# Performance work log

Measured on AMD Instinct MI355X. Metric: run time of the kernel, lower is better.

The kernel has to match this reference:

```python
import jax, jax.numpy as jnp
import numpy as np

B, T, D, H, L = 64, 512, 256, 512, 4


def setup_inputs() -> dict:
    key = jax.random.key(0)
    ks = jax.random.split(key, 1 + 2 * L)
    inp = {"x": jax.random.normal(ks[0], (B, T, D), dtype=jnp.float32)}
    s = 0.05
    for l in range(L):
        in_dim = D if l == 0 else H
        inp[f"W{l}"] = jax.random.normal(ks[1 + 2 * l], (4 * H, in_dim), dtype=jnp.float32) * s
        inp[f"U{l}"] = jax.random.normal(ks[2 + 2 * l], (4 * H, H), dtype=jnp.float32) * s
        inp[f"bw{l}"] = jnp.zeros((4 * H,), dtype=jnp.float32)
        inp[f"bu{l}"] = jnp.zeros((4 * H,), dtype=jnp.float32)
    return inp


def _lstm_forward(x, params):
    # x: [B, T, D]; params: list of (W [4H,in], U [4H,H], bw [4H], bu [4H])
    Bq = x.shape[0]
    h0 = [jnp.zeros((Bq, H), x.dtype) for _ in range(L)]
    c0 = [jnp.zeros((Bq, H), x.dtype) for _ in range(L)]

    def step(carry, x_t):
        hs, cs = carry
        new_h, new_c = [], []
        inp = x_t  # [B, in]
        for (W, U, bw, bu), h_i, c_i in zip(params, hs, cs):
            z = inp @ W.T + bw + h_i @ U.T + bu  # [B, 4H]
            f, i, o, g = jnp.split(z, 4, axis=-1)  # gate order f,i,o,g
            f = jax.nn.sigmoid(f)
            i = jax.nn.sigmoid(i)
            o = jax.nn.sigmoid(o)
            g = jnp.tanh(g)
            c_n = f * c_i + i * g
            h_n = o * jnp.tanh(c_n)
            new_h.append(h_n)
            new_c.append(c_n)
            inp = h_n
        return (new_h, new_c), inp

    (h_f, c_f), out = jax.lax.scan(step, (h0, c0), jnp.swapaxes(x, 0, 1))
    output = jnp.swapaxes(out, 0, 1)  # [B, T, H]
    return output, jnp.stack(h_f), jnp.stack(c_f)


def reference(x, W0, U0, bw0, bu0, W1, U1, bw1, bu1, W2, U2, bw2, bu2, W3, U3, bw3, bu3):
    params = [(W0, U0, bw0, bu0), (W1, U1, bw1, bu1), (W2, U2, bw2, bu2), (W3, U3, bw3, bu3)]
    return _lstm_forward(x, params)
```

## Files before the change

kernel.cpp:

```cpp
#include <hip/hip_runtime.h>

typedef __attribute__((ext_vector_type(8))) short bf16x8;
typedef __attribute__((ext_vector_type(4))) float f32x4;

#define WPL 32
#define NT 256
#define RING 8

__device__ __forceinline__ unsigned short f2bf(float f) {
  unsigned int u = __float_as_uint(f);
  u += 0x7FFFu + ((u >> 16) & 1u);
  return (unsigned short)(u >> 16);
}
__device__ __forceinline__ float sigmoid_fast(float x) {
  return __builtin_amdgcn_rcpf(1.0f + __builtin_amdgcn_exp2f(-1.4426950408889634f * x));
}
__device__ __forceinline__ float tanh_fast(float x) {
  return 1.0f - 2.0f * __builtin_amdgcn_rcpf(
                           1.0f + __builtin_amdgcn_exp2f(2.885390081777927f * x));
}
__device__ __forceinline__ void wait_vm0() {
  asm volatile("s_waitcnt vmcnt(0)" ::: "memory");
  __builtin_amdgcn_sched_barrier(0);
}
#define WAITVM(N)                                         \
  do {                                                    \
    asm volatile("s_waitcnt vmcnt(" #N ")" ::: "memory"); \
    __builtin_amdgcn_sched_barrier(0);                    \
  } while (0)

template <int MODE>
__device__ __forceinline__ void ldA(bf16x8& d, int voff, const unsigned short* base) {
  if constexpr (MODE == 0)
    asm volatile("global_load_dwordx4 %0, %1, %2"
                 : "=v"(d) : "v"(voff), "s"(base));
  else
    asm volatile("global_load_dwordx4 %0, %1, %2 sc0 sc1"
                 : "=v"(d) : "v"(voff), "s"(base));
}
__device__ __forceinline__ unsigned ld_flag(const unsigned* p) {
  unsigned v;
  asm volatile("global_load_dword %0, %1, off sc0 sc1\n\ts_waitcnt vmcnt(0)"
               : "=v"(v) : "v"(p) : "memory");
  return v;
}
__device__ __forceinline__ void st16_coh(void* p, f32x4 v) {
  asm volatile("global_store_dwordx4 %0, %1, off sc0 sc1" :: "v"(p), "v"(v) : "memory");
}
__device__ __forceinline__ void st4_coh(void* p, unsigned v) {
  asm volatile("global_store_dword %0, %1, off sc0 sc1" :: "v"(p), "v"(v) : "memory");
}


__global__ void cvt_x_kernel(const float* __restrict__ x,
                             unsigned short* __restrict__ xf) {
  int tid = blockIdx.x * 256 + threadIdx.x;
  int t     = tid >> 11;
  int inner = tid & 2047;
  int lane  = inner & 63;
  int bt    = (inner >> 6) & 3;
  int c     = inner >> 8;
  int b = bt * 16 + (lane & 15);
  int d = c * 32 + (lane >> 4) * 8;
  const float* s = x + ((size_t)b * 512 + t) * 256 + d;
  f32x4 v0 = *(const f32x4*)s;
  f32x4 v1 = *(const f32x4*)(s + 4);
  bf16x8 o;
  o[0] = (short)f2bf(v0[0]); o[1] = (short)f2bf(v0[1]);
  o[2] = (short)f2bf(v0[2]); o[3] = (short)f2bf(v0[3]);
  o[4] = (short)f2bf(v1[0]); o[5] = (short)f2bf(v1[1]);
  o[6] = (short)f2bf(v1[2]); o[7] = (short)f2bf(v1[3]);
  *(bf16x8*)(xf + (size_t)t * 16384 + (size_t)inner * 8) = o;
}

__global__ void cvt_w_kernel(const float* __restrict__ W,
                             const float* __restrict__ U,
                             unsigned short* __restrict__ dst,
                             int C2, int split) {
  int tid = blockIdx.x * 256 + threadIdx.x;
  int lane = tid & 63;
  int c    = (tid >> 6) % C2;
  int rest = tid / (64 * C2);
  int g = rest & 3;
  int w = rest >> 2;
  int row = g * 512 + w * 16 + (lane & 15);
  int k   = c * 32 + (lane >> 4) * 8;
  const float* s = (k < split) ? (W + (size_t)row * split + k)
                               : (U + (size_t)row * 512 + (k - split));
  f32x4 v0 = *(const f32x4*)s;
  f32x4 v1 = *(const f32x4*)(s + 4);
  bf16x8 o;
  o[0] = (short)f2bf(v0[0]); o[1] = (short)f2bf(v0[1]);
  o[2] = (short)f2bf(v0[2]); o[3] = (short)f2bf(v0[3]);
  o[4] = (short)f2bf(v1[0]); o[5] = (short)f2bf(v1[1]);
  o[6] = (short)f2bf(v1[2]); o[7] = (short)f2bf(v1[3]);
  *(bf16x8*)(dst + (size_t)tid * 8) = o;
}

__global__ void bias_kernel(const float* __restrict__ bw,
                            const float* __restrict__ bu,
                            float* __restrict__ dst) {
  int i = blockIdx.x * 256 + threadIdx.x;
  dst[i] = bw[i] + bu[i];
}

__global__ void zero_flags(unsigned int* __restrict__ p) {
  int i = blockIdx.x * 256 + threadIdx.x;
  p[i] = 0u;
}

template <int C1, int C2, int M1, int M2>
__device__ __forceinline__ void gemm_run(const unsigned short* __restrict__ a1,
                                         const unsigned short* __restrict__ a2,
                                         const char* bg0, const char* bg1,
                                         const char* bg2, const char* bg3,
                                         int voffA, f32x4 acc[4]) {
  constexpr int NP = C2 / 4;
  bf16x8 av[3][4];
  bf16x8 bb[2][4][4];
  const char* bgp[4] = {bg0, bg1, bg2, bg3};

  auto issueA_iter = [&](int cc, int s3, int i) {
    if (cc < C1)
      ldA<M1>(av[s3][i], voffA + cc * 4096, a1);
    else
      ldA<M2>(av[s3][i], voffA + (cc - C1) * 4096, a2);
  };
  auto issueA_phase = [&](int q) {
#pragma unroll
    for (int i = 0; i < 4; ++i) issueA_iter(4 * q + i, q % 3, i);
  };
  auto loadB_phase = [&](int q) {
#pragma unroll
    for (int i = 0; i < 4; ++i)
#pragma unroll
      for (int g = 0; g < 4; ++g)
        bb[q & 1][i][g] = *(const bf16x8*)(bgp[g] + (4 * q + i) * 1024);
  };

#pragma unroll
  for (int q = 0; q < 3; ++q)
    if (q < NP) issueA_phase(q);
  loadB_phase(0);

#pragma unroll
  for (int ph = 0; ph < NP; ++ph) {
    if (ph + 1 < NP) loadB_phase(ph + 1);
    if (ph < NP - 2) {
      WAITVM(8);
    } else if (ph == NP - 2) {
      WAITVM(4);
    } else {
      WAITVM(0);
    }
#pragma unroll
    for (int i = 0; i < 4; ++i)
#pragma unroll
      for (int g = 0; g < 4; ++g)
        acc[g] = __builtin_amdgcn_mfma_f32_16x16x32_bf16(av[ph % 3][i],
                                                         bb[ph & 1][i][g],
                                                         acc[g], 0, 0, 0);
    if (ph + 3 < NP) issueA_phase(ph + 3);
  }
}

__global__ void __launch_bounds__(NT, 1)
lstm_main(const unsigned short* __restrict__ xfrag,
          const unsigned short* __restrict__ wf0,
          const unsigned short* __restrict__ wf1,
          const unsigned short* __restrict__ wf2,
          const unsigned short* __restrict__ wf3,
          const float* __restrict__ bias,
          unsigned short* __restrict__ hbuf,
          unsigned int* __restrict__ flags,
          float* __restrict__ out) {
  extern __shared__ char smem[];

  const int bid   = blockIdx.x;
  const int layer = bid >> 5;
  const int w     = bid & 31;
  const int tid   = threadIdx.x;
  const int lane  = tid & 63;
  const int vm    = tid >> 6;
  const int l15   = lane & 15;
  const int lhi   = lane >> 4;
  const int hcol  = w * 16 + l15;
  const int C2r   = (layer == 0) ? 24 : 32;
  const int HOFF  = 4 * C2r * 64 * 16;

  const unsigned short* wfl =
      (layer == 0) ? wf0 : (layer == 1) ? wf1 : (layer == 2) ? wf2 : wf3;
  const unsigned short* wsl = wfl + (size_t)w * (4 * C2r * 64 * 8);

  for (int i = tid; i < 4 * C2r * 64; i += NT)
    *(f32x4*)(smem + (size_t)i * 16) = *(const f32x4*)(wsl + (size_t)i * 8);
  __syncthreads();

  const char* bg[4];
#pragma unroll
  for (int g = 0; g < 4; ++g) bg[g] = smem + ((size_t)g * C2r * 64 + lane) * 16;

  float bv[4];
#pragma unroll
  for (int g = 0; g < 4; ++g) bv[g] = bias[layer * 2048 + g * 512 + hcol];

  float creg[4];
#pragma unroll
  for (int r = 0; r < 4; ++r) creg[r] = 0.f;

  const int voffA = lane * 16 + vm * 1024;
  const int base_w = (w >> 1) * 2048 + (w & 1) * 256;

  const unsigned short* hprev =
      (layer == 0) ? nullptr : (hbuf + (size_t)(layer - 1) * RING * 32768);
  const unsigned short* hself = hbuf + (size_t)layer * RING * 32768;

  const int sb_bt = tid >> 5;
  const int sb_q  = (tid >> 4) & 1;
  const int sb_bl = tid & 15;
  const int slot_off = base_w + sb_bt * 512 + sb_q * 128 + sb_bl * 8;

  if (layer > 0 && vm == 0) {
    const unsigned* fp = flags;
    unsigned need = 0;
    if (lane < 32) {
      fp = flags + ((layer - 1) * 32 + lane) * 16;
      need = 1u;
    }
    while (true) {
      unsigned v = need ? ld_flag(fp) : 0u;
      if (__ballot(need && v < need) == 0) break;
      __builtin_amdgcn_s_sleep(1);
    }
  }
  __syncthreads();
  wait_vm0();

  for (int t = 0; t < 512; ++t) {
    const unsigned short* aW =
        (layer == 0) ? (xfrag + (size_t)t * 16384)
                     : (hprev + (size_t)(t & (RING - 1)) * 32768);
    const unsigned short* aU =
        hself + (size_t)((t - 1) & (RING - 1)) * 32768;

    f32x4 acc[4];
    const f32x4 z4 = {0.f, 0.f, 0.f, 0.f};
#pragma unroll
    for (int g = 0; g < 4; ++g) acc[g] = z4;

    if (t == 0) {
      if (layer == 0)
        gemm_run<8, 8, 0, 0>(aW, aW, bg[0], bg[1], bg[2], bg[3], voffA, acc);
      else
        gemm_run<16, 16, 2, 2>(aW, aW, bg[0], bg[1], bg[2], bg[3], voffA, acc);
    } else {
      if (layer == 0)
        gemm_run<8, 24, 0, 2>(aW, aU, bg[0], bg[1], bg[2], bg[3], voffA, acc);
      else
        gemm_run<16, 32, 2, 2>(aW, aU, bg[0], bg[1], bg[2], bg[3], voffA, acc);
    }

    float hreg[4], cnreg[4];
#pragma unroll
    for (int r = 0; r < 4; ++r) {
      float fg = sigmoid_fast(acc[0][r] + bv[0]);
      float ig = sigmoid_fast(acc[1][r] + bv[1]);
      float og = sigmoid_fast(acc[2][r] + bv[2]);
      float gg = tanh_fast(acc[3][r] + bv[3]);
      float cn = fg * creg[r] + ig * gg;
      creg[r] = cn;
      cnreg[r] = cn;
      float h = og * tanh_fast(cn);
      hreg[r] = h;
      *(unsigned short*)(smem + HOFF + (vm * 16 + lhi * 4 + r) * 32 + l15 * 2) =
          f2bf(h);
    }
    __syncthreads();

    if (tid < 128) {
      f32x4 hv = *(const f32x4*)(smem + HOFF + (sb_bt * 16 + sb_bl) * 32 + sb_q * 16);
      unsigned short* dst = hbuf +
          ((size_t)layer * RING + (t & (RING - 1))) * 32768 + slot_off;
      st16_coh(dst, hv);
      wait_vm0();
    }
    __syncthreads();
    if (tid == 0)
      st4_coh(flags + (layer * 32 + w) * 16, (unsigned)(t + 1));

    if (layer == 3) {
#pragma unroll
      for (int r = 0; r < 4; ++r) {
        int bidx = vm * 16 + lhi * 4 + r;
        out[(size_t)bidx * 262144 + (size_t)t * 512 + hcol] = hreg[r];
      }
    }
    if (t == 511) {
#pragma unroll
      for (int r = 0; r < 4; ++r) {
        int bidx = vm * 16 + lhi * 4 + r;
        out[16777216 + ((size_t)layer * 64 + bidx) * 512 + hcol] = hreg[r];
        out[16777216 + 131072 + ((size_t)layer * 64 + bidx) * 512 + hcol] = cnreg[r];
      }
    }

    if (t < 511) {
      if (vm == 0) {
        const unsigned* fp = flags;
        unsigned need = 0;
        if (lane < 32) {
          if (layer > 0) {
            fp = flags + ((layer - 1) * 32 + lane) * 16;
            need = (unsigned)(t + 2);
          }
        } else {
          fp = flags + (layer * 32 + (lane - 32)) * 16;
          need = (unsigned)(t + 1);
        }
        while (true) {
          unsigned v = need ? ld_flag(fp) : 0u;
          if (__ballot(need && v < need) == 0) break;
          __builtin_amdgcn_s_sleep(1);
        }
      } else if (vm == 1) {
        const unsigned* fp = flags;
        unsigned need = 0;
        if (lane < 32 && layer < 3 && (t + 1) >= RING) {
          fp = flags + ((layer + 1) * 32 + lane) * 16;
          need = (unsigned)(t + 2 - RING);
        }
        while (true) {
          unsigned v = need ? ld_flag(fp) : 0u;
          if (__ballot(need && v < need) == 0) break;
          __builtin_amdgcn_s_sleep(1);
        }
      }
      __syncthreads();
      wait_vm0();
    }
  }
}

extern "C" void kernel_launch(void* const* d_in, const int* in_sizes, int n_in,
                              void* d_out, int out_size, void* d_ws, size_t ws_size,
                              hipStream_t stream) {
  const float* x = (const float*)d_in[0];
  const float *W[4], *U[4], *bw[4], *bu[4];
  for (int l = 0; l < 4; ++l) {
    W[l]  = (const float*)d_in[1 + 4 * l];
    U[l]  = (const float*)d_in[2 + 4 * l];
    bw[l] = (const float*)d_in[3 + 4 * l];
    bu[l] = (const float*)d_in[4 + 4 * l];
  }

  char* ws = (char*)d_ws;
  unsigned short* xfrag = (unsigned short*)(ws + 0);
  unsigned short* wfr0  = (unsigned short*)(ws + 16777216);
  unsigned short* wfr1  = (unsigned short*)(ws + 19922944);
  unsigned short* wfr2  = (unsigned short*)(ws + 24117248);
  unsigned short* wfr3  = (unsigned short*)(ws + 28311552);
  float*          biasp = (float*)(ws + 32505856);
  unsigned short* hbuf  = (unsigned short*)(ws + 32538624);
  unsigned int*   flags = (unsigned int*)(ws + 34635776);
  float* out = (float*)d_out;

  cvt_x_kernel<<<4096, 256, 0, stream>>>(x, xfrag);
  cvt_w_kernel<<<768, 256, 0, stream>>>(W[0], U[0], wfr0, 24, 256);
  cvt_w_kernel<<<1024, 256, 0, stream>>>(W[1], U[1], wfr1, 32, 512);
  cvt_w_kernel<<<1024, 256, 0, stream>>>(W[2], U[2], wfr2, 32, 512);
  cvt_w_kernel<<<1024, 256, 0, stream>>>(W[3], U[3], wfr3, 32, 512);
  bias_kernel<<<8, 256, 0, stream>>>(bw[0], bu[0], biasp + 0 * 2048);
  bias_kernel<<<8, 256, 0, stream>>>(bw[1], bu[1], biasp + 1 * 2048);
  bias_kernel<<<8, 256, 0, stream>>>(bw[2], bu[2], biasp + 2 * 2048);
  bias_kernel<<<8, 256, 0, stream>>>(bw[3], bu[3], biasp + 3 * 2048);
  zero_flags<<<8, 256, 0, stream>>>(flags);

  hipFuncSetAttribute((const void*)lstm_main,
                      hipFuncAttributeMaxDynamicSharedMemorySize, 135168);
  lstm_main<<<dim3(4 * WPL), dim3(NT), 135168, stream>>>(
      xfrag, wfr0, wfr1, wfr2, wfr3, biasp, hbuf, flags, out);
}
```

Baseline: 1.891 ms.

## Halve block to two waves, each computing two 16-row M tiles

Cuts threads per block from 256 to 128, so each wave covers two 16-row batch tiles and reuses every LDS-loaded B fragment across two MFMAs. Per-wave LDS weight reads are roughly halved relative to compute, and block-wide syncs involve fewer waves on this latency-bound recurrent step. In exchange each wave does twice the MFMA and activation work per step with less parallelism to hide latency, and register pressure rises from the doubled accumulators and cell state.

```diff
diff --git a/kernel.cpp b/kernel.cpp
--- a/kernel.cpp
+++ b/kernel.cpp
@@ -4,7 +4,7 @@
 typedef __attribute__((ext_vector_type(4))) float f32x4;
 
 #define WPL 32
-#define NT 256
+#define NT 128
 #define RING 8
 
 __device__ __forceinline__ unsigned short f2bf(float f) {
@@ -114,28 +114,32 @@
                                          const unsigned short* __restrict__ a2,
                                          const char* bg0, const char* bg1,
                                          const char* bg2, const char* bg3,
-                                         int voffA, f32x4 acc[4]) {
-  constexpr int NP = C2 / 4;
-  bf16x8 av[3][4];
-  bf16x8 bb[2][4][4];
+                                         int voffA, f32x4 acc[2][4]) {
+  constexpr int NP = C2 / 2;
+  bf16x8 av[3][2][2];
+  bf16x8 bb[2][2][4];
   const char* bgp[4] = {bg0, bg1, bg2, bg3};
 
-  auto issueA_iter = [&](int cc, int s3, int i) {
-    if (cc < C1)
-      ldA<M1>(av[s3][i], voffA + cc * 4096, a1);
-    else
-      ldA<M2>(av[s3][i], voffA + (cc - C1) * 4096, a2);
-  };
   auto issueA_phase = [&](int q) {
 #pragma unroll
-    for (int i = 0; i < 4; ++i) issueA_iter(4 * q + i, q % 3, i);
+    for (int kk = 0; kk < 2; ++kk) {
+      int cc = 2 * q + kk;
+#pragma unroll
+      for (int m = 0; m < 2; ++m) {
+        int vo = voffA + m * 1024;
+        if (cc < C1)
+          ldA<M1>(av[q % 3][kk][m], vo + cc * 4096, a1);
+        else
+          ldA<M2>(av[q % 3][kk][m], vo + (cc - C1) * 4096, a2);
+      }
+    }
   };
   auto loadB_phase = [&](int q) {
 #pragma unroll
-    for (int i = 0; i < 4; ++i)
+    for (int kk = 0; kk < 2; ++kk)
 #pragma unroll
       for (int g = 0; g < 4; ++g)
-        bb[q & 1][i][g] = *(const bf16x8*)(bgp[g] + (4 * q + i) * 1024);
+        bb[q & 1][kk][g] = *(const bf16x8*)(bgp[g] + (2 * q + kk) * 1024);
   };
 
 #pragma unroll
@@ -154,12 +158,14 @@
       WAITVM(0);
     }
 #pragma unroll
-    for (int i = 0; i < 4; ++i)
-#pragma unroll
-      for (int g = 0; g < 4; ++g)
-        acc[g] = __builtin_amdgcn_mfma_f32_16x16x32_bf16(av[ph % 3][i],
-                                                         bb[ph & 1][i][g],
-                                                         acc[g], 0, 0, 0);
+    for (int kk = 0; kk < 2; ++kk)
+#pragma unroll
+      for (int g = 0; g < 4; ++g) {
+        acc[0][g] = __builtin_amdgcn_mfma_f32_16x16x32_bf16(
+            av[ph % 3][kk][0], bb[ph & 1][kk][g], acc[0][g], 0, 0, 0);
+        acc[1][g] = __builtin_amdgcn_mfma_f32_16x16x32_bf16(
+            av[ph % 3][kk][1], bb[ph & 1][kk][g], acc[1][g], 0, 0, 0);
+      }
     if (ph + 3 < NP) issueA_phase(ph + 3);
   }
 }
@@ -204,11 +210,13 @@
 #pragma unroll
   for (int g = 0; g < 4; ++g) bv[g] = bias[layer * 2048 + g * 512 + hcol];
 
-  float creg[4];
-#pragma unroll
-  for (int r = 0; r < 4; ++r) creg[r] = 0.f;
-
-  const int voffA = lane * 16 + vm * 1024;
+  float creg[2][4];
+#pragma unroll
+  for (int m = 0; m < 2; ++m)
+#pragma unroll
+    for (int r = 0; r < 4; ++r) creg[m][r] = 0.f;
+
+  const int voffA = lane * 16 + vm * 2048;
   const int base_w = (w >> 1) * 2048 + (w & 1) * 256;
 
   const unsigned short* hprev =
@@ -243,10 +251,12 @@
     const unsigned short* aU =
         hself + (size_t)((t - 1) & (RING - 1)) * 32768;
 
-    f32x4 acc[4];
+    f32x4 acc[2][4];
     const f32x4 z4 = {0.f, 0.f, 0.f, 0.f};
 #pragma unroll
-    for (int g = 0; g < 4; ++g) acc[g] = z4;
+    for (int m = 0; m < 2; ++m)
+#pragma unroll
+      for (int g = 0; g < 4; ++g) acc[m][g] = z4;
 
     if (t == 0) {
       if (layer == 0)
@@ -260,24 +270,27 @@
         gemm_run<16, 32, 2, 2>(aW, aU, bg[0], bg[1], bg[2], bg[3], voffA, acc);
     }
 
-    float hreg[4], cnreg[4];
-#pragma unroll
-    for (int r = 0; r < 4; ++r) {
-      float fg = sigmoid_fast(acc[0][r] + bv[0]);
-      float ig = sigmoid_fast(acc[1][r] + bv[1]);
-      float og = sigmoid_fast(acc[2][r] + bv[2]);
-      float gg = tanh_fast(acc[3][r] + bv[3]);
-      float cn = fg * creg[r] + ig * gg;
-      creg[r] = cn;
-      cnreg[r] = cn;
-      float h = og * tanh_fast(cn);
-      hreg[r] = h;
-      *(unsigned short*)(smem + HOFF + (vm * 16 + lhi * 4 + r) * 32 + l15 * 2) =
-          f2bf(h);
+    float hreg[2][4], cnreg[2][4];
+#pragma unroll
+    for (int m = 0; m < 2; ++m) {
+#pragma unroll
+      for (int r = 0; r < 4; ++r) {
+        float fg = sigmoid_fast(acc[m][0][r] + bv[0]);
+        float ig = sigmoid_fast(acc[m][1][r] + bv[1]);
+        float og = sigmoid_fast(acc[m][2][r] + bv[2]);
+        float gg = tanh_fast(acc[m][3][r] + bv[3]);
+        float cn = fg * creg[m][r] + ig * gg;
+        creg[m][r] = cn;
+        cnreg[m][r] = cn;
+        float h = og * tanh_fast(cn);
+        hreg[m][r] = h;
+        int row = vm * 32 + m * 16 + lhi * 4 + r;
+        *(unsigned short*)(smem + HOFF + row * 32 + l15 * 2) = f2bf(h);
+      }
     }
     __syncthreads();
 
-    if (tid < 128) {
+    {
       f32x4 hv = *(const f32x4*)(smem + HOFF + (sb_bt * 16 + sb_bl) * 32 + sb_q * 16);
       unsigned short* dst = hbuf +
           ((size_t)layer * RING + (t & (RING - 1))) * 32768 + slot_off;
@@ -290,18 +303,23 @@
 
     if (layer == 3) {
 #pragma unroll
-      for (int r = 0; r < 4; ++r) {
-        int bidx = vm * 16 + lhi * 4 + r;
-        out[(size_t)bidx * 262144 + (size_t)t * 512 + hcol] = hreg[r];
-      }
+      for (int m = 0; m < 2; ++m)
+#pragma unroll
+        for (int r = 0; r < 4; ++r) {
+          int bidx = vm * 32 + m * 16 + lhi * 4 + r;
+          out[(size_t)bidx * 262144 + (size_t)t * 512 + hcol] = hreg[m][r];
+        }
     }
     if (t == 511) {
 #pragma unroll
-      for (int r = 0; r < 4; ++r) {
-        int bidx = vm * 16 + lhi * 4 + r;
-        out[16777216 + ((size_t)layer * 64 + bidx) * 512 + hcol] = hreg[r];
-        out[16777216 + 131072 + ((size_t)layer * 64 + bidx) * 512 + hcol] = cnreg[r];
-      }
+      for (int m = 0; m < 2; ++m)
+#pragma unroll
+        for (int r = 0; r < 4; ++r) {
+          int bidx = vm * 32 + m * 16 + lhi * 4 + r;
+          out[16777216 + ((size_t)layer * 64 + bidx) * 512 + hcol] = hreg[m][r];
+          out[16777216 + 131072 + ((size_t)layer * 64 + bidx) * 512 + hcol] =
+              cnreg[m][r];
+        }
     }
 
     if (t < 511) {
@@ -322,7 +340,7 @@
           if (__ballot(need && v < need) == 0) break;
           __builtin_amdgcn_s_sleep(1);
         }
-      } else if (vm == 1) {
+      } else {
         const unsigned* fp = flags;
         unsigned need = 0;
         if (lane < 32 && layer < 3 && (t + 1) >= RING) {
```

New measurement: 2.413 ms. 27.6% more time.

## Switch LSTM recurrence GEMM to 32x32x16 MFMA with LDS-staged gate epilogue

Applied to the files above, without the earlier changes.

Replaces the four 16x16x32 MFMAs per k-step (one per gate) with a single 32x32x16 bf16 MFMA per wave. The four waves are arranged as a 2x2 tile of batch by gate-row, and the x and weight fragment layouts are rewritten to match. Because each thread no longer holds all four gates, accumulators are staged through LDS and 128 threads compute the gate nonlinearities, producing vectorized h stores and output writes. The aim is fewer MFMA instructions and fewer B-fragment LDS reads per step. The cost is an extra LDS round trip plus synchronization on the serial critical path, and LDS use grows.

```diff
diff --git a/kernel.cpp b/kernel.cpp
--- a/kernel.cpp
+++ b/kernel.cpp
@@ -2,6 +2,7 @@
 
 typedef __attribute__((ext_vector_type(8))) short bf16x8;
 typedef __attribute__((ext_vector_type(4))) float f32x4;
+typedef __attribute__((ext_vector_type(16))) float f32x16;
 
 #define WPL 32
 #define NT 256
@@ -58,10 +59,10 @@
   int t     = tid >> 11;
   int inner = tid & 2047;
   int lane  = inner & 63;
-  int bt    = (inner >> 6) & 3;
-  int c     = inner >> 8;
-  int b = bt * 16 + (lane & 15);
-  int d = c * 32 + (lane >> 4) * 8;
+  int vm    = (inner >> 6) & 1;
+  int ks    = inner >> 7;
+  int b = vm * 32 + (lane & 31);
+  int d = ks * 16 + (lane >> 5) * 8;
   const float* s = x + ((size_t)b * 512 + t) * 256 + d;
   f32x4 v0 = *(const f32x4*)s;
   f32x4 v1 = *(const f32x4*)(s + 4);
@@ -81,10 +82,11 @@
   int lane = tid & 63;
   int c    = (tid >> 6) % C2;
   int rest = tid / (64 * C2);
-  int g = rest & 3;
-  int w = rest >> 2;
-  int row = g * 512 + w * 16 + (lane & 15);
-  int k   = c * 32 + (lane >> 4) * 8;
+  int vn = rest & 1;
+  int w  = rest >> 1;
+  int zz = vn * 32 + (lane & 31);
+  int row = (zz >> 4) * 512 + w * 16 + (zz & 15);
+  int k   = c * 16 + (lane >> 5) * 8;
   const float* s = (k < split) ? (W + (size_t)row * split + k)
                                : (U + (size_t)row * 512 + (k - split));
   f32x4 v0 = *(const f32x4*)s;
@@ -112,30 +114,25 @@
 template <int C1, int C2, int M1, int M2>
 __device__ __forceinline__ void gemm_run(const unsigned short* __restrict__ a1,
                                          const unsigned short* __restrict__ a2,
-                                         const char* bg0, const char* bg1,
-                                         const char* bg2, const char* bg3,
-                                         int voffA, f32x4 acc[4]) {
+                                         const char* bg, int voffA, f32x16& acc) {
   constexpr int NP = C2 / 4;
   bf16x8 av[3][4];
-  bf16x8 bb[2][4][4];
-  const char* bgp[4] = {bg0, bg1, bg2, bg3};
-
-  auto issueA_iter = [&](int cc, int s3, int i) {
-    if (cc < C1)
-      ldA<M1>(av[s3][i], voffA + cc * 4096, a1);
-    else
-      ldA<M2>(av[s3][i], voffA + (cc - C1) * 4096, a2);
-  };
+  bf16x8 bb[2][4];
+
   auto issueA_phase = [&](int q) {
 #pragma unroll
-    for (int i = 0; i < 4; ++i) issueA_iter(4 * q + i, q % 3, i);
+    for (int i = 0; i < 4; ++i) {
+      int cc = 4 * q + i;
+      if (cc < C1)
+        ldA<M1>(av[q % 3][i], voffA + cc * 2048, a1);
+      else
+        ldA<M2>(av[q % 3][i], voffA + (cc - C1) * 2048, a2);
+    }
   };
   auto loadB_phase = [&](int q) {
 #pragma unroll
     for (int i = 0; i < 4; ++i)
-#pragma unroll
-      for (int g = 0; g < 4; ++g)
-        bb[q & 1][i][g] = *(const bf16x8*)(bgp[g] + (4 * q + i) * 1024);
+      bb[q & 1][i] = *(const bf16x8*)(bg + (4 * q + i) * 1024);
   };
 
 #pragma unroll
@@ -155,11 +152,8 @@
     }
 #pragma unroll
     for (int i = 0; i < 4; ++i)
-#pragma unroll
-      for (int g = 0; g < 4; ++g)
-        acc[g] = __builtin_amdgcn_mfma_f32_16x16x32_bf16(av[ph % 3][i],
-                                                         bb[ph & 1][i][g],
-                                                         acc[g], 0, 0, 0);
+      acc = __builtin_amdgcn_mfma_f32_32x32x16_bf16(av[ph % 3][i],
+                                                    bb[ph & 1][i], acc, 0, 0, 0);
     if (ph + 3 < NP) issueA_phase(ph + 3);
   }
 }
@@ -181,46 +175,50 @@
   const int w     = bid & 31;
   const int tid   = threadIdx.x;
   const int lane  = tid & 63;
-  const int vm    = tid >> 6;
-  const int l15   = lane & 15;
-  const int lhi   = lane >> 4;
-  const int hcol  = w * 16 + l15;
-  const int C2r   = (layer == 0) ? 24 : 32;
-  const int HOFF  = 4 * C2r * 64 * 16;
+  const int wv    = tid >> 6;
+  const int vm    = wv & 1;
+  const int vn    = wv >> 1;
+  const int C2r   = (layer == 0) ? 48 : 64;
+  const int HOFF  = 2 * C2r * 64 * 16;
 
   const unsigned short* wfl =
       (layer == 0) ? wf0 : (layer == 1) ? wf1 : (layer == 2) ? wf2 : wf3;
-  const unsigned short* wsl = wfl + (size_t)w * (4 * C2r * 64 * 8);
-
-  for (int i = tid; i < 4 * C2r * 64; i += NT)
+  const unsigned short* wsl = wfl + (size_t)w * (2 * C2r * 64 * 8);
+
+  for (int i = tid; i < 2 * C2r * 64; i += NT)
     *(f32x4*)(smem + (size_t)i * 16) = *(const f32x4*)(wsl + (size_t)i * 8);
   __syncthreads();
 
-  const char* bg[4];
-#pragma unroll
-  for (int g = 0; g < 4; ++g) bg[g] = smem + ((size_t)g * C2r * 64 + lane) * 16;
-
-  float bv[4];
-#pragma unroll
-  for (int g = 0; g < 4; ++g) bv[g] = bias[layer * 2048 + g * 512 + hcol];
-
-  float creg[4];
-#pragma unroll
-  for (int r = 0; r < 4; ++r) creg[r] = 0.f;
+  const char* bg = smem + ((size_t)vn * C2r * 64 + lane) * 16;
+  float* ztf = (float*)(smem + HOFF);
+
+  const int pvm   = tid >> 6;
+  const int plane = tid & 63;
+  const int eb    = pvm * 32 + (plane & 31);
+  const int ehc8  = (plane >> 5) * 8;
+
+  f32x4 bv4[4][2];
+#pragma unroll
+  for (int g = 0; g < 4; ++g) {
+    const float* bp = bias + layer * 2048 + g * 512 + w * 16 + ehc8;
+    bv4[g][0] = *(const f32x4*)bp;
+    bv4[g][1] = *(const f32x4*)(bp + 4);
+  }
+
+  float creg[8];
+#pragma unroll
+  for (int r = 0; r < 8; ++r) creg[r] = 0.f;
 
   const int voffA = lane * 16 + vm * 1024;
-  const int base_w = (w >> 1) * 2048 + (w & 1) * 256;
 
   const unsigned short* hprev =
       (layer == 0) ? nullptr : (hbuf + (size_t)(layer - 1) * RING * 32768);
   const unsigned short* hself = hbuf + (size_t)layer * RING * 32768;
 
-  const int sb_bt = tid >> 5;
-  const int sb_q  = (tid >> 4) & 1;
-  const int sb_bl = tid & 15;
-  const int slot_off = base_w + sb_bt * 512 + sb_q * 128 + sb_bl * 8;
-
-  if (layer > 0 && vm == 0) {
+  const int zz    = vn * 32 + (lane & 31);
+  const int rbase = vm * 32 + 4 * (lane >> 5);
+
+  if (layer > 0 && wv == 0) {
     const unsigned* fp = flags;
     unsigned need = 0;
     if (lane < 32) {
@@ -243,69 +241,82 @@
     const unsigned short* aU =
         hself + (size_t)((t - 1) & (RING - 1)) * 32768;
 
-    f32x4 acc[4];
-    const f32x4 z4 = {0.f, 0.f, 0.f, 0.f};
-#pragma unroll
-    for (int g = 0; g < 4; ++g) acc[g] = z4;
+    f32x16 acc = {};
 
     if (t == 0) {
       if (layer == 0)
-        gemm_run<8, 8, 0, 0>(aW, aW, bg[0], bg[1], bg[2], bg[3], voffA, acc);
+        gemm_run<16, 16, 0, 0>(aW, aW, bg, voffA, acc);
       else
-        gemm_run<16, 16, 2, 2>(aW, aW, bg[0], bg[1], bg[2], bg[3], voffA, acc);
+        gemm_run<32, 32, 2, 2>(aW, aW, bg, voffA, acc);
     } else {
       if (layer == 0)
-        gemm_run<8, 24, 0, 2>(aW, aU, bg[0], bg[1], bg[2], bg[3], voffA, acc);
+        gemm_run<16, 48, 0, 2>(aW, aU, bg, voffA, acc);
       else
-        gemm_run<16, 32, 2, 2>(aW, aU, bg[0], bg[1], bg[2], bg[3], voffA, acc);
-    }
-
-    float hreg[4], cnreg[4];
-#pragma unroll
-    for (int r = 0; r < 4; ++r) {
-      float fg = sigmoid_fast(acc[0][r] + bv[0]);
-      float ig = sigmoid_fast(acc[1][r] + bv[1]);
-      float og = sigmoid_fast(acc[2][r] + bv[2]);
-      float gg = tanh_fast(acc[3][r] + bv[3]);
-      float cn = fg * creg[r] + ig * gg;
-      creg[r] = cn;
-      cnreg[r] = cn;
-      float h = og * tanh_fast(cn);
-      hreg[r] = h;
-      *(unsigned short*)(smem + HOFF + (vm * 16 + lhi * 4 + r) * 32 + l15 * 2) =
-          f2bf(h);
+        gemm_run<32, 64, 2, 2>(aW, aU, bg, voffA, acc);
+    }
+
+#pragma unroll
+    for (int rg = 0; rg < 4; ++rg) {
+      f32x4 v = {acc[4 * rg], acc[4 * rg + 1], acc[4 * rg + 2], acc[4 * rg + 3]};
+      *(f32x4*)(ztf + zz * 68 + rbase + 8 * rg) = v;
     }
     __syncthreads();
 
+    float hreg[8], cnreg[8];
     if (tid < 128) {
-      f32x4 hv = *(const f32x4*)(smem + HOFF + (sb_bt * 16 + sb_bl) * 32 + sb_q * 16);
+      bf16x8 hb;
+#pragma unroll
+      for (int e = 0; e < 8; ++e) {
+        int hc = ehc8 + e;
+        float bf_ = (e < 4) ? bv4[0][0][e] : bv4[0][1][e - 4];
+        float bi_ = (e < 4) ? bv4[1][0][e] : bv4[1][1][e - 4];
+        float bo_ = (e < 4) ? bv4[2][0][e] : bv4[2][1][e - 4];
+        float bg_ = (e < 4) ? bv4[3][0][e] : bv4[3][1][e - 4];
+        float fg = sigmoid_fast(ztf[(0 + hc) * 68 + eb] + bf_);
+        float ig = sigmoid_fast(ztf[(16 + hc) * 68 + eb] + bi_);
+        float og = sigmoid_fast(ztf[(32 + hc) * 68 + eb] + bo_);
+        float gg = tanh_fast(ztf[(48 + hc) * 68 + eb] + bg_);
+        float cn = fg * creg[e] + ig * gg;
+        creg[e] = cn;
+        cnreg[e] = cn;
+        float h = og * tanh_fast(cn);
+        hreg[e] = h;
+        hb[e] = (short)f2bf(h);
+      }
       unsigned short* dst = hbuf +
-          ((size_t)layer * RING + (t & (RING - 1))) * 32768 + slot_off;
-      st16_coh(dst, hv);
+          ((size_t)layer * RING + (t & (RING - 1))) * 32768 +
+          w * 1024 + pvm * 512 + plane * 8;
+      st16_coh(dst, __builtin_bit_cast(f32x4, hb));
       wait_vm0();
     }
     __syncthreads();
     if (tid == 0)
       st4_coh(flags + (layer * 32 + w) * 16, (unsigned)(t + 1));
 
-    if (layer == 3) {
-#pragma unroll
-      for (int r = 0; r < 4; ++r) {
-        int bidx = vm * 16 + lhi * 4 + r;
-        out[(size_t)bidx * 262144 + (size_t)t * 512 + hcol] = hreg[r];
+    if (tid < 128) {
+      if (layer == 3) {
+        float* op = out + (size_t)eb * 262144 + (size_t)t * 512 + w * 16 + ehc8;
+        f32x4 h0 = {hreg[0], hreg[1], hreg[2], hreg[3]};
+        f32x4 h1 = {hreg[4], hreg[5], hreg[6], hreg[7]};
+        *(f32x4*)op = h0;
+        *(f32x4*)(op + 4) = h1;
       }
-    }
-    if (t == 511) {
-#pragma unroll
-      for (int r = 0; r < 4; ++r) {
-        int bidx = vm * 16 + lhi * 4 + r;
-        out[16777216 + ((size_t)layer * 64 + bidx) * 512 + hcol] = hreg[r];
-        out[16777216 + 131072 + ((size_t)layer * 64 + bidx) * 512 + hcol] = cnreg[r];
+      if (t == 511) {
+        float* hp = out + 16777216 + ((size_t)layer * 64 + eb) * 512 + w * 16 + ehc8;
+        float* cp = hp + 131072;
+        f32x4 h0 = {hreg[0], hreg[1], hreg[2], hreg[3]};
+        f32x4 h1 = {hreg[4], hreg[5], hreg[6], hreg[7]};
+        f32x4 c0 = {cnreg[0], cnreg[1], cnreg[2], cnreg[3]};
+        f32x4 c1 = {cnreg[4], cnreg[5], cnreg[6], cnreg[7]};
+        *(f32x4*)hp = h0;
+        *(f32x4*)(hp + 4) = h1;
+        *(f32x4*)cp = c0;
+        *(f32x4*)(cp + 4) = c1;
       }
     }
 
     if (t < 511) {
-      if (vm == 0) {
+      if (wv == 0) {
         const unsigned* fp = flags;
         unsigned need = 0;
         if (lane < 32) {
@@ -322,7 +333,7 @@
           if (__ballot(need && v < need) == 0) break;
           __builtin_amdgcn_s_sleep(1);
         }
-      } else if (vm == 1) {
+      } else if (wv == 1) {
         const unsigned* fp = flags;
         unsigned need = 0;
         if (lane < 32 && layer < 3 && (t + 1) >= RING) {
@@ -365,10 +376,10 @@
   float* out = (float*)d_out;
 
   cvt_x_kernel<<<4096, 256, 0, stream>>>(x, xfrag);
-  cvt_w_kernel<<<768, 256, 0, stream>>>(W[0], U[0], wfr0, 24, 256);
-  cvt_w_kernel<<<1024, 256, 0, stream>>>(W[1], U[1], wfr1, 32, 512);
-  cvt_w_kernel<<<1024, 256, 0, stream>>>(W[2], U[2], wfr2, 32, 512);
-  cvt_w_kernel<<<1024, 256, 0, stream>>>(W[3], U[3], wfr3, 32, 512);
+  cvt_w_kernel<<<768, 256, 0, stream>>>(W[0], U[0], wfr0, 48, 256);
+  cvt_w_kernel<<<1024, 256, 0, stream>>>(W[1], U[1], wfr1, 64, 512);
+  cvt_w_kernel<<<1024, 256, 0, stream>>>(W[2], U[2], wfr2, 64, 512);
+  cvt_w_kernel<<<1024, 256, 0, stream>>>(W[3], U[3], wfr3, 64, 512);
   bias_kernel<<<8, 256, 0, stream>>>(bw[0], bu[0], biasp + 0 * 2048);
   bias_kernel<<<8, 256, 0, stream>>>(bw[1], bu[1], biasp + 1 * 2048);
   bias_kernel<<<8, 256, 0, stream>>>(bw[2], bu[2], biasp + 2 * 2048);
@@ -376,7 +387,7 @@
   zero_flags<<<8, 256, 0, stream>>>(flags);
 
   hipFuncSetAttribute((const void*)lstm_main,
-                      hipFuncAttributeMaxDynamicSharedMemorySize, 135168);
-  lstm_main<<<dim3(4 * WPL), dim3(NT), 135168, stream>>>(
+                      hipFuncAttributeMaxDynamicSharedMemorySize, 148480);
+  lstm_main<<<dim3(4 * WPL), dim3(NT), 148480, stream>>>(
       xfrag, wfr0, wfr1, wfr2, wfr3, biasp, hbuf, flags, out);
 }
```

New measurement: 2.490 ms. 1.32x slower.
